# Performance work log

Measured on AMD Instinct MI355X. Metric: run time of the kernel, lower is better.

Reference implementation:

```python
import jax, jax.numpy as jnp
import numpy as np

N_ENTITIES = 100000
N_USERS = 50000
CHANNEL = 64
N_RELATIONS = 16
N_FACTORS = 4
N_EDGES = 1600000
N_INTER = 1000000


def setup_inputs() -> dict:
    key = jax.random.key(0)
    ks = jax.random.split(key, 11)
    return {
        "entity_emb": jax.random.normal(ks[0], (N_ENTITIES, CHANNEL), dtype=jnp.float32),
        "user_emb": jax.random.normal(ks[1], (N_USERS, CHANNEL), dtype=jnp.float32),
        "latent_emb": jax.random.normal(ks[2], (N_FACTORS, CHANNEL), dtype=jnp.float32),
        "weight": jax.random.normal(ks[3], (N_RELATIONS, CHANNEL), dtype=jnp.float32),
        "disen_weight_att": jax.random.normal(ks[4], (N_FACTORS, N_RELATIONS), dtype=jnp.float32),
        "interact_vals": jax.random.uniform(ks[5], (N_INTER,), dtype=jnp.float32),
        "head": jax.random.randint(ks[6], (N_EDGES,), 0, N_ENTITIES),
        "tail": jax.random.randint(ks[7], (N_EDGES,), 0, N_ENTITIES),
        # edge_type is 1-indexed in the original (weight[edge_type - 1])
        "edge_type": jax.random.randint(ks[8], (N_EDGES,), 1, N_RELATIONS + 1),
        "interact_rows": jax.random.randint(ks[9], (N_INTER,), 0, N_USERS),
        "interact_cols": jax.random.randint(ks[10], (N_INTER,), 0, N_ENTITIES),
    }


def reference(entity_emb, user_emb, latent_emb, weight, disen_weight_att,
              interact_vals, head, tail, edge_type, interact_rows, interact_cols):
    # ---- KG aggregate (GATED_ATT branch, vectorized; chunk loop is math-identical) ----
    rel = weight[edge_type - 1]                                  # [E, C]
    att = jax.nn.sigmoid(jnp.sum(entity_emb[head] * rel, axis=1))[:, None]  # [E, 1]
    neigh = att * (entity_emb[tail] * rel)                       # [E, C]
    seg_sum = jax.ops.segment_sum(neigh, head, num_segments=N_ENTITIES)     # [N_e, C]
    cnt = jax.ops.segment_sum(jnp.ones_like(att[:, 0]), head, num_segments=N_ENTITIES)
    entity_agg = seg_sum / jnp.maximum(cnt, 1.0)[:, None]        # scatter_mean (0 if empty)

    # ---- user aggregate ----
    score = jax.nn.softmax(user_emb @ latent_emb.T, axis=1)[:, :, None]      # [U, F, 1]
    user_agg = jax.ops.segment_sum(interact_vals[:, None] * entity_emb[interact_cols],
                                   interact_rows, num_segments=N_USERS)      # sparse mm
    disen = jax.nn.softmax(disen_weight_att, axis=-1) @ weight               # [F, C]
    gate = jnp.sum(disen[None, :, :] * score, axis=1)                        # [U, C]
    user_agg = user_agg * gate + user_agg
    return entity_agg, user_agg
```

## Files before the change

### kernel.cpp

```cpp
#include <hip/hip_runtime.h>

#define N_ENTITIES 100000
#define N_USERS 50000
#define CHANNEL 64
#define N_RELATIONS 16
#define N_FACTORS 4
#define N_EDGES 1600000
#define N_INTER 1000000
#define TMASK ((1 << 17) - 1)

#define BSH 6
#define BSZ 64
#define NBE 1563
#define NBU 782
#define CAP_E 1536
#define CAP_U 1792
#define TILE_E 4096
#define TILE_U 4096
#define NCONV 6250

typedef unsigned short u16;

__device__ __forceinline__ float wave_reduce_sum(float p) {
    #pragma unroll
    for (int off = 32; off > 0; off >>= 1) p += __shfl_xor(p, off);
    return p;
}

__device__ __forceinline__ int block_scan_incl(int v, int* wsum) {
    int lane = threadIdx.x & 63, wid = threadIdx.x >> 6;
    int x = v;
    #pragma unroll
    for (int off = 1; off < 64; off <<= 1) {
        int y = __shfl_up(x, off);
        if (lane >= off) x += y;
    }
    __syncthreads();
    if (lane == 63) wsum[wid] = x;
    __syncthreads();
    if (wid == 0) {
        int s = (lane < 16) ? wsum[lane] : 0;
        #pragma unroll
        for (int off = 1; off < 16; off <<= 1) {
            int y = __shfl_up(s, off);
            if (lane >= off) s += y;
        }
        if (lane < 16) wsum[lane] = s;
    }
    __syncthreads();
    return x + (wid ? wsum[wid - 1] : 0);
}

__device__ __forceinline__ u16 f32_to_bf16_rne(float x) {
    unsigned u = __float_as_uint(x);
    return (u16)((u + 0x7FFFu + ((u >> 16) & 1u)) >> 16);
}

template <bool BF16>
__device__ __forceinline__ float ldrow(const float* __restrict__ e32,
                                       const u16* __restrict__ e16,
                                       int row, int lane) {
    if (BF16) return __uint_as_float(((unsigned)e16[(size_t)row * CHANNEL + lane]) << 16);
    return e32[(size_t)row * CHANNEL + lane];
}

__device__ __forceinline__ void disen_body(const float* __restrict__ dwa,
                                           const float* __restrict__ weight,
                                           float* __restrict__ disen) {
    int f = threadIdx.x >> 6;
    int c = threadIdx.x & 63;
    float m = -INFINITY;
    #pragma unroll
    for (int r = 0; r < N_RELATIONS; ++r) m = fmaxf(m, dwa[f * N_RELATIONS + r]);
    float denom = 0.f, acc = 0.f;
    #pragma unroll
    for (int r = 0; r < N_RELATIONS; ++r) {
        float e = expf(dwa[f * N_RELATIONS + r] - m);
        denom += e;
        acc += e * weight[r * CHANNEL + c];
    }
    disen[f * CHANNEL + c] = acc / denom;
}

__global__ void disen_kernel(const float* __restrict__ dwa,
                             const float* __restrict__ weight,
                             float* __restrict__ disen) {
    disen_body(dwa, weight, disen);
}

__global__ __launch_bounds__(256) void conv_disen_kernel(
    const float* __restrict__ src, u16* __restrict__ dst,
    const float* __restrict__ dwa, const float* __restrict__ weight,
    float* __restrict__ disen) {
    if (blockIdx.x == NCONV) { disen_body(dwa, weight, disen); return; }
    int i = blockIdx.x * 256 + threadIdx.x;
    float4 v = ((const float4*)src)[i];
    ushort4 o;
    o.x = f32_to_bf16_rne(v.x);
    o.y = f32_to_bf16_rne(v.y);
    o.z = f32_to_bf16_rne(v.z);
    o.w = f32_to_bf16_rne(v.w);
    ((ushort4*)dst)[i] = o;
}

__global__ __launch_bounds__(1024) void hist_kernel(
    const int* __restrict__ head, const int* __restrict__ irows,
    int* __restrict__ wp_e, int* __restrict__ wp_u) {
    __shared__ int lh[NBE + NBU];
    int tid = threadIdx.x;
    for (int i = tid; i < NBE + NBU; i += 1024) lh[i] = 0;
    __syncthreads();
    const int NTOT = N_EDGES + N_INTER;
    for (int i = blockIdx.x * 1024 + tid; i < NTOT; i += gridDim.x * 1024) {
        if (i < N_EDGES) atomicAdd(&lh[head[i] >> BSH], 1);
        else             atomicAdd(&lh[NBE + (irows[i - N_EDGES] >> BSH)], 1);
    }
    __syncthreads();
    for (int i = tid; i < NBE + NBU; i += 1024) {
        int c = lh[i];
        if (c) {
            if (i < NBE) atomicAdd(&wp_e[i], c);
            else         atomicAdd(&wp_u[i - NBE], c);
        }
    }
}

__global__ __launch_bounds__(1024) void scan_kernel(
    int* __restrict__ wp_e, int* __restrict__ coff_e,
    int* __restrict__ wp_u, int* __restrict__ coff_u) {
    __shared__ int wsum[16];
    int tid = threadIdx.x;
    int c0 = wp_e[tid];
    int incl0 = block_scan_incl(c0, wsum);
    int tot0 = wsum[15];
    int i1 = 1024 + tid;
    int c1 = (i1 < NBE) ? wp_e[i1] : 0;
    int incl1 = block_scan_incl(c1, wsum) + tot0;
    int cu = (tid < NBU) ? wp_u[tid] : 0;
    int inclu = block_scan_incl(cu, wsum);
    { int ex = incl0 - c0; coff_e[tid] = ex; wp_e[tid] = ex; }
    if (i1 < NBE) { int ex = incl1 - c1; coff_e[i1] = ex; wp_e[i1] = ex; }
    if (tid == 0) coff_e[NBE] = N_EDGES;
    if (tid < NBU) { int ex = inclu - cu; coff_u[tid] = ex; wp_u[tid] = ex; }
    if (tid == 0) coff_u[NBU] = N_INTER;
}

__global__ __launch_bounds__(1024) void scatter_edge_kernel(
    const int* __restrict__ head, const int* __restrict__ tail,
    const int* __restrict__ etype,
    int* __restrict__ wp, int* __restrict__ pay_g) {
    __shared__ int s_hist[NBE], s_lofs[NBE], s_gbase[NBE];
    __shared__ int s_pay[TILE_E];
    __shared__ int s_dest[TILE_E];
    __shared__ int wsum[16];
    int tid = threadIdx.x;
    int g0 = blockIdx.x * TILE_E;
    int tilecnt = min(TILE_E, N_EDGES - g0);
    for (int i = tid; i < NBE; i += 1024) s_hist[i] = 0;
    int cb[4], pp[4], rk[4];
    __syncthreads();
    #pragma unroll
    for (int j = 0; j < 4; ++j) {
        int s = j * 1024 + tid;
        if (s < tilecnt) {
            int i = g0 + s;
            int h = head[i];
            cb[j] = h >> BSH;
            pp[j] = ((h & (BSZ - 1)) << 21) | ((etype[i] - 1) << 17) | tail[i];
        } else cb[j] = -1;
    }
    #pragma unroll
    for (int j = 0; j < 4; ++j)
        if (cb[j] >= 0) rk[j] = atomicAdd(&s_hist[cb[j]], 1);
    __syncthreads();
    int c0 = s_hist[tid];
    int incl0 = block_scan_incl(c0, wsum);
    int tot0 = wsum[15];
    int i1 = 1024 + tid;
    int c1 = (i1 < NBE) ? s_hist[i1] : 0;
    int incl1 = block_scan_incl(c1, wsum) + tot0;
    {
        int ex = incl0 - c0;
        s_lofs[tid] = ex;
        if (c0 > 0) s_gbase[tid] = atomicAdd(&wp[tid], c0) - ex;
    }
    if (i1 < NBE) {
        int ex = incl1 - c1;
        s_lofs[i1] = ex;
        if (c1 > 0) s_gbase[i1] = atomicAdd(&wp[i1], c1) - ex;
    }
    __syncthreads();
    #pragma unroll
    for (int j = 0; j < 4; ++j) {
        if (cb[j] >= 0) {
            int slot = s_lofs[cb[j]] + rk[j];
            s_pay[slot]  = pp[j];
            s_dest[slot] = s_gbase[cb[j]] + slot;
        }
    }
    __syncthreads();
    #pragma unroll
    for (int j = 0; j < 4; ++j) {
        int s = j * 1024 + tid;
        if (s < tilecnt) pay_g[s_dest[s]] = s_pay[s];
    }
}

__global__ __launch_bounds__(1024) void scatter_inter_kernel(
    const int* __restrict__ irows, const int* __restrict__ icols,
    const float* __restrict__ vals,
    int* __restrict__ wp, int* __restrict__ payA_g, float* __restrict__ payB_g) {
    __shared__ int s_hist[NBU], s_lofs[NBU], s_gbase[NBU];
    __shared__ int s_pay[TILE_U];
    __shared__ float s_val[TILE_U];
    __shared__ int s_dest[TILE_U];
    __shared__ int wsum[16];
    int tid = threadIdx.x;
    int g0 = blockIdx.x * TILE_U;
    int tilecnt = min(TILE_U, N_INTER - g0);
    for (int i = tid; i < NBU; i += 1024) s_hist[i] = 0;
    int cb[4], pp[4], rk[4];
    float vv[4];
    __syncthreads();
    #pragma unroll
    for (int j = 0; j < 4; ++j) {
        int s = j * 1024 + tid;
        if (s < tilecnt) {
            int i = g0 + s;
            int u = irows[i];
            cb[j] = u >> BSH;
            pp[j] = ((u & (BSZ - 1)) << 17) | icols[i];
            vv[j] = vals[i];
        } else cb[j] = -1;
    }
    #pragma unroll
    for (int j = 0; j < 4; ++j)
        if (cb[j] >= 0) rk[j] = atomicAdd(&s_hist[cb[j]], 1);
    __syncthreads();
    int c0 = (tid < NBU) ? s_hist[tid] : 0;
    int incl0 = block_scan_incl(c0, wsum);
    if (tid < NBU) {
        int ex = incl0 - c0;
        s_lofs[tid] = ex;
        if (c0 > 0) s_gbase[tid] = atomicAdd(&wp[tid], c0) - ex;
    }
    __syncthreads();
    #pragma unroll
    for (int j = 0; j < 4; ++j) {
        if (cb[j] >= 0) {
            int slot = s_lofs[cb[j]] + rk[j];
            s_pay[slot]  = pp[j];
            s_val[slot]  = vv[j];
            s_dest[slot] = s_gbase[cb[j]] + slot;
        }
    }
    __syncthreads();
    #pragma unroll
    for (int j = 0; j < 4; ++j) {
        int s = j * 1024 + tid;
        if (s < tilecnt) {
            payA_g[s_dest[s]] = s_pay[s];
            payB_g[s_dest[s]] = s_val[s];
        }
    }
}

template <bool BF16>
__global__ __launch_bounds__(256, 8) void gather_kernel(
    const float* __restrict__ entity_emb,
    const u16* __restrict__ emb16,
    const float* __restrict__ weight,
    const float* __restrict__ user_emb,
    const float* __restrict__ latent_emb,
    const float* __restrict__ disen,
    const int* __restrict__ coff_e,
    const int* __restrict__ pay_e,
    const int* __restrict__ coff_u,
    const int* __restrict__ payA_u,
    const float* __restrict__ payB_u,
    float* __restrict__ entity_agg,
    float* __restrict__ user_agg) {
    __shared__ __align__(16) char smem[16896];
    int tid = threadIdx.x;
    int wv = tid >> 6, lane = tid & 63;
    int bid = blockIdx.x;

    if (bid < NBE) {
        float* w65    = (float*)smem;
        float* s_attv = w65 + 1040;
        int*   s_pay  = (int*)(s_attv + 1024);
        int*   s_hist = s_pay + CAP_E;
        int*   s_scan = s_hist + 64;

        for (int i = tid; i < N_RELATIONS * CHANNEL; i += 256)
            w65[(i >> 6) * 65 + (i & 63)] = weight[i];
        if (tid < BSZ) s_hist[tid] = 0;
        int kbeg = coff_e[bid];
        int n = min(coff_e[bid + 1] - kbeg, CAP_E);
        __syncthreads();

        int myp[CAP_E / 256], myr[CAP_E / 256];
        #pragma unroll
        for (int j = 0; j < CAP_E / 256; ++j) {
            int s = j * 256 + tid;
            if (s < n) {
                int p = pay_e[kbeg + s];
                myp[j] = p;
                myr[j] = atomicAdd(&s_hist[p >> 21], 1);
            }
        }
        __syncthreads();
        if (wv == 0) {
            int x = s_hist[lane];
            #pragma unroll
            for (int off = 1; off < 64; off <<= 1) {
                int y = __shfl_up(x, off);
                if (lane >= off) x += y;
            }
            s_scan[lane] = x;
        }
        __syncthreads();
        #pragma unroll
        for (int j = 0; j < CAP_E / 256; ++j) {
            int s = j * 256 + tid;
            if (s < n) {
                int key = myp[j] >> 21;
                s_pay[s_scan[key] - s_hist[key] + myr[j]] = myp[j];
            }
        }

        int r = lane >> 2, q = lane & 3;
        for (int t = 0; t < 16; ++t) {
            int le = wv * 16 + t;
            int ge = bid * BSZ + le;
            if (ge >= N_ENTITIES) break;
            float eh = entity_emb[(size_t)ge * CHANNEL + lane];
            float p = 0.f;
            #pragma unroll
            for (int j = 0; j < 16; ++j)
                p += __shfl(eh, q * 16 + j) * w65[r * 65 + q * 16 + j];
            p += __shfl_xor(p, 1);
            p += __shfl_xor(p, 2);
            if (q == 0) s_attv[(le << 4) + r] = 1.f / (1.f + expf(-p));
        }
        __syncthreads();

        #define EBODY(K) { \
            int pp = s_pay[K]; \
            int et = (pp >> 17) & 15; \
            float v = ldrow<BF16>(entity_emb, emb16, pp & TMASK, lane); \
            acc += s_attv[(le << 4) + et] * v * w65[et * 65 + lane]; }
        for (int t = 0; t < 16; ++t) {
            int le = wv * 16 + t;
            int ge = bid * BSZ + le;
            if (ge >= N_ENTITIES) break;
            int cnt = s_hist[le];
            int ke = s_scan[le];
            int k = ke - cnt;
            float acc = 0.f;
            for (; k + 4 <= ke; k += 4) {
                EBODY(k); EBODY(k + 1); EBODY(k + 2); EBODY(k + 3);
            }
            for (; k < ke; ++k) EBODY(k);
            entity_agg[(size_t)ge * CHANNEL + lane] = acc / fmaxf((float)cnt, 1.0f);
        }
        #undef EBODY
    } else {
        int*   s_pay  = (int*)smem;
        float* s_val  = (float*)(s_pay + CAP_U);
        float* s_lat  = s_val + CAP_U;
        float* s_dis  = s_lat + 256;
        int*   s_hist = (int*)(s_dis + 256);
        int*   s_scan = s_hist + 64;

        if (tid < BSZ) s_hist[tid] = 0;
        if (tid < N_FACTORS * CHANNEL) {
            s_lat[tid] = latent_emb[tid];
            s_dis[tid] = disen[tid];
        }
        int b = bid - NBE;
        int kbeg = coff_u[b];
        int n = min(coff_u[b + 1] - kbeg, CAP_U);
        __syncthreads();

        int myp[CAP_U / 256], myr[CAP_U / 256];
        float myv[CAP_U / 256];
        #pragma unroll
        for (int j = 0; j < CAP_U / 256; ++j) {
            int s = j * 256 + tid;
            if (s < n) {
                int p = payA_u[kbeg + s];
                myp[j] = p;
                myv[j] = payB_u[kbeg + s];
                myr[j] = atomicAdd(&s_hist[p >> 17], 1);
            }
        }
        __syncthreads();
        if (wv == 0) {
            int x = s_hist[lane];
            #pragma unroll
            for (int off = 1; off < 64; off <<= 1) {
                int y = __shfl_up(x, off);
                if (lane >= off) x += y;
            }
            s_scan[lane] = x;
        }
        __syncthreads();
        #pragma unroll
        for (int j = 0; j < CAP_U / 256; ++j) {
            int s = j * 256 + tid;
            if (s < n) {
                int key = myp[j] >> 17;
                int slot = s_scan[key] - s_hist[key] + myr[j];
                s_pay[slot] = myp[j] & TMASK;
                s_val[slot] = myv[j];
            }
        }
        __syncthreads();

        #define UBODY(K) { \
            float v = ldrow<BF16>(entity_emb, emb16, s_pay[K], lane); \
            acc += s_val[K] * v; }
        for (int t = 0; t < 16; ++t) {
            int lu = wv * 16 + t;
            int gu = b * BSZ + lu;
            if (gu >= N_USERS) break;
            int cnt = s_hist[lu];
            int ke = s_scan[lu];
            int k = ke - cnt;
            float acc = 0.f;
            for (; k + 4 <= ke; k += 4) {
                UBODY(k); UBODY(k + 1); UBODY(k + 2); UBODY(k + 3);
            }
            for (; k < ke; ++k) UBODY(k);

            float ue = user_emb[(size_t)gu * CHANNEL + lane];
            float s[N_FACTORS];
            #pragma unroll
            for (int f = 0; f < N_FACTORS; ++f)
                s[f] = wave_reduce_sum(ue * s_lat[f * CHANNEL + lane]);
            float m = fmaxf(fmaxf(s[0], s[1]), fmaxf(s[2], s[3]));
            float d = 0.f;
            #pragma unroll
            for (int f = 0; f < N_FACTORS; ++f) { s[f] = expf(s[f] - m); d += s[f]; }
            float gate = 0.f;
            #pragma unroll
            for (int f = 0; f < N_FACTORS; ++f)
                gate += s_dis[f * CHANNEL + lane] * (s[f] / d);
            user_agg[(size_t)gu * CHANNEL + lane] = acc * gate + acc;
        }
        #undef UBODY
    }
}

extern "C" void kernel_launch(void* const* d_in, const int* in_sizes, int n_in,
                              void* d_out, int out_size, void* d_ws, size_t ws_size,
                              hipStream_t stream) {
    const float* entity_emb    = (const float*)d_in[0];
    const float* user_emb      = (const float*)d_in[1];
    const float* latent_emb    = (const float*)d_in[2];
    const float* weight        = (const float*)d_in[3];
    const float* dwa           = (const float*)d_in[4];
    const float* interact_vals = (const float*)d_in[5];
    const int*   head          = (const int*)d_in[6];
    const int*   tail          = (const int*)d_in[7];
    const int*   edge_type     = (const int*)d_in[8];
    const int*   irows         = (const int*)d_in[9];
    const int*   icols         = (const int*)d_in[10];

    float* entity_agg = (float*)d_out;
    float* user_agg   = (float*)d_out + (size_t)N_ENTITIES * CHANNEL;

    int*   wp_e   = (int*)d_ws;
    int*   wp_u   = wp_e + NBE;
    int*   coff_e = wp_u + NBU;
    int*   coff_u = coff_e + NBE + 1;
    int*   pay_e  = coff_u + NBU + 1;
    int*   payA_u = pay_e + N_EDGES;
    float* payB_u = (float*)(payA_u + N_INTER);
    float* disen  = payB_u + N_INTER;
    u16*   emb16  = (u16*)(disen + N_FACTORS * CHANNEL);

    size_t need_bf16 = (size_t)((char*)(emb16 + (size_t)N_ENTITIES * CHANNEL) - (char*)d_ws);
    bool use_bf16 = (ws_size >= need_bf16);
    if (!use_bf16) emb16 = (u16*)d_ws;

    hipMemsetAsync(wp_e, 0, (size_t)(NBE + NBU) * sizeof(int), stream);

    if (use_bf16) {
        conv_disen_kernel<<<NCONV + 1, 256, 0, stream>>>(
            entity_emb, emb16, dwa, weight, disen);
    } else {
        disen_kernel<<<1, 256, 0, stream>>>(dwa, weight, disen);
    }

    hist_kernel<<<128, 1024, 0, stream>>>(head, irows, wp_e, wp_u);
    scan_kernel<<<1, 1024, 0, stream>>>(wp_e, coff_e, wp_u, coff_u);

    scatter_edge_kernel<<<(N_EDGES + TILE_E - 1) / TILE_E, 1024, 0, stream>>>(
        head, tail, edge_type, wp_e, pay_e);
    scatter_inter_kernel<<<(N_INTER + TILE_U - 1) / TILE_U, 1024, 0, stream>>>(
        irows, icols, interact_vals, wp_u, payA_u, payB_u);

    if (use_bf16) {
        gather_kernel<true><<<NBE + NBU, 256, 0, stream>>>(
            entity_emb, emb16, weight, user_emb, latent_emb, disen,
            coff_e, pay_e, coff_u, payA_u, payB_u, entity_agg, user_agg);
    } else {
        gather_kernel<false><<<NBE + NBU, 256, 0, stream>>>(
            entity_emb, emb16, weight, user_emb, latent_emb, disen,
            coff_e, pay_e, coff_u, payA_u, payB_u, entity_agg, user_agg);
    }
}
```

Baseline: 201.2 us.

## Sort gather payloads by source-row chunk and fuse histogram into prep kernel

Inside each gather block, payloads are now bucketed by (source-entity chunk, destination row) instead of destination row alone. The gather loop walks the four 25000-row chunks in order, keeping 16 per-row accumulators in registers, so rows that are gathered concurrently fall in a narrower address range and should hit L2 more often. Separately, the histogram pass is merged into the bf16 conversion and disen kernel, which removes one launch. The cost is a 256-bucket scan, payloads read twice from global memory, more shared memory, and higher register pressure from the accumulator array.

```diff
diff --git a/kernel.cpp b/kernel.cpp
--- a/kernel.cpp
+++ b/kernel.cpp
@@ -18,6 +18,9 @@
 #define TILE_E 4096
 #define TILE_U 4096
 #define NCONV 6250
+#define NHIST 256
+#define NCHUNK 4
+#define CHUNK_ROWS 25000
 
 typedef unsigned short u16;
 
@@ -64,6 +67,27 @@
     return e32[(size_t)row * CHANNEL + lane];
 }
 
+__device__ __forceinline__ void scan256(const int* s_hist, int* s_scan,
+                                        int* s_wp, int* wtot) {
+    int tid = threadIdx.x;
+    int lane = tid & 63, wv = tid >> 6;
+    int c = s_hist[tid];
+    int x = c;
+    #pragma unroll
+    for (int off = 1; off < 64; off <<= 1) {
+        int y = __shfl_up(x, off);
+        if (lane >= off) x += y;
+    }
+    if (lane == 63) wtot[wv] = x;
+    __syncthreads();
+    if (wv >= 1) x += wtot[0];
+    if (wv >= 2) x += wtot[1];
+    if (wv >= 3) x += wtot[2];
+    s_scan[tid] = x;
+    s_wp[tid]   = x - c;
+    __syncthreads();
+}
+
 __device__ __forceinline__ void disen_body(const float* __restrict__ dwa,
                                            const float* __restrict__ weight,
                                            float* __restrict__ disen) {
@@ -88,19 +112,43 @@
     disen_body(dwa, weight, disen);
 }
 
-__global__ __launch_bounds__(256) void conv_disen_kernel(
+__global__ __launch_bounds__(256) void prep_kernel(
     const float* __restrict__ src, u16* __restrict__ dst,
     const float* __restrict__ dwa, const float* __restrict__ weight,
-    float* __restrict__ disen) {
-    if (blockIdx.x == NCONV) { disen_body(dwa, weight, disen); return; }
-    int i = blockIdx.x * 256 + threadIdx.x;
-    float4 v = ((const float4*)src)[i];
-    ushort4 o;
-    o.x = f32_to_bf16_rne(v.x);
-    o.y = f32_to_bf16_rne(v.y);
-    o.z = f32_to_bf16_rne(v.z);
-    o.w = f32_to_bf16_rne(v.w);
-    ((ushort4*)dst)[i] = o;
+    float* __restrict__ disen,
+    const int* __restrict__ head, const int* __restrict__ irows,
+    int* __restrict__ wp_e, int* __restrict__ wp_u) {
+    __shared__ int lh[NBE + NBU];
+    int bid = blockIdx.x;
+    int tid = threadIdx.x;
+    if (bid < NCONV) {
+        int i = bid * 256 + tid;
+        float4 v = ((const float4*)src)[i];
+        ushort4 o;
+        o.x = f32_to_bf16_rne(v.x);
+        o.y = f32_to_bf16_rne(v.y);
+        o.z = f32_to_bf16_rne(v.z);
+        o.w = f32_to_bf16_rne(v.w);
+        ((ushort4*)dst)[i] = o;
+        return;
+    }
+    if (bid == NCONV) { disen_body(dwa, weight, disen); return; }
+    for (int i = tid; i < NBE + NBU; i += 256) lh[i] = 0;
+    __syncthreads();
+    const int NTOT = N_EDGES + N_INTER;
+    int hb = bid - NCONV - 1;
+    for (int i = hb * 256 + tid; i < NTOT; i += NHIST * 256) {
+        if (i < N_EDGES) atomicAdd(&lh[head[i] >> BSH], 1);
+        else             atomicAdd(&lh[NBE + (irows[i - N_EDGES] >> BSH)], 1);
+    }
+    __syncthreads();
+    for (int i = tid; i < NBE + NBU; i += 256) {
+        int c = lh[i];
+        if (c) {
+            if (i < NBE) atomicAdd(&wp_e[i], c);
+            else         atomicAdd(&wp_u[i - NBE], c);
+        }
+    }
 }
 
 __global__ __launch_bounds__(1024) void hist_kernel(
@@ -280,7 +328,7 @@
     const float* __restrict__ payB_u,
     float* __restrict__ entity_agg,
     float* __restrict__ user_agg) {
-    __shared__ __align__(16) char smem[16896];
+    __shared__ __align__(16) char smem[19520];
     int tid = threadIdx.x;
     int wv = tid >> 6, lane = tid & 63;
     int bid = blockIdx.x;
@@ -290,43 +338,28 @@
         float* s_attv = w65 + 1040;
         int*   s_pay  = (int*)(s_attv + 1024);
         int*   s_hist = s_pay + CAP_E;
-        int*   s_scan = s_hist + 64;
+        int*   s_scan = s_hist + 256;
+        int*   s_wp   = s_scan + 256;
+        int*   wtot   = s_wp + 256;
 
         for (int i = tid; i < N_RELATIONS * CHANNEL; i += 256)
             w65[(i >> 6) * 65 + (i & 63)] = weight[i];
-        if (tid < BSZ) s_hist[tid] = 0;
+        s_hist[tid] = 0;
         int kbeg = coff_e[bid];
         int n = min(coff_e[bid + 1] - kbeg, CAP_E);
         __syncthreads();
 
-        int myp[CAP_E / 256], myr[CAP_E / 256];
-        #pragma unroll
-        for (int j = 0; j < CAP_E / 256; ++j) {
-            int s = j * 256 + tid;
-            if (s < n) {
-                int p = pay_e[kbeg + s];
-                myp[j] = p;
-                myr[j] = atomicAdd(&s_hist[p >> 21], 1);
-            }
+        for (int s = tid; s < n; s += 256) {
+            int p = pay_e[kbeg + s];
+            int key = ((int)((unsigned)(p & TMASK) / CHUNK_ROWS) << 6) | (p >> 21);
+            atomicAdd(&s_hist[key], 1);
         }
         __syncthreads();
-        if (wv == 0) {
-            int x = s_hist[lane];
-            #pragma unroll
-            for (int off = 1; off < 64; off <<= 1) {
-                int y = __shfl_up(x, off);
-                if (lane >= off) x += y;
-            }
-            s_scan[lane] = x;
-        }
-        __syncthreads();
-        #pragma unroll
-        for (int j = 0; j < CAP_E / 256; ++j) {
-            int s = j * 256 + tid;
-            if (s < n) {
-                int key = myp[j] >> 21;
-                s_pay[s_scan[key] - s_hist[key] + myr[j]] = myp[j];
-            }
+        scan256(s_hist, s_scan, s_wp, wtot);
+        for (int s = tid; s < n; s += 256) {
+            int p = pay_e[kbeg + s];
+            int key = ((int)((unsigned)(p & TMASK) / CHUNK_ROWS) << 6) | (p >> 21);
+            s_pay[atomicAdd(&s_wp[key], 1)] = p;
         }
 
         int r = lane >> 2, q = lane & 3;
@@ -345,35 +378,62 @@
         }
         __syncthreads();
 
-        #define EBODY(K) { \
-            int pp = s_pay[K]; \
-            int et = (pp >> 17) & 15; \
-            float v = ldrow<BF16>(entity_emb, emb16, pp & TMASK, lane); \
-            acc += s_attv[(le << 4) + et] * v * w65[et * 65 + lane]; }
+        float acc[16];
+        #pragma unroll
+        for (int t = 0; t < 16; ++t) acc[t] = 0.f;
+
+        for (int c = 0; c < NCHUNK; ++c) {
+            #pragma unroll
+            for (int t = 0; t < 16; ++t) {
+                int le = wv * 16 + t;
+                int key = (c << 6) | le;
+                int ke = s_scan[key];
+                int k = ke - s_hist[key];
+                float a = acc[t];
+                for (; k + 4 <= ke; k += 4) {
+                    int p0 = s_pay[k], p1 = s_pay[k + 1];
+                    int p2 = s_pay[k + 2], p3 = s_pay[k + 3];
+                    float v0 = ldrow<BF16>(entity_emb, emb16, p0 & TMASK, lane);
+                    float v1 = ldrow<BF16>(entity_emb, emb16, p1 & TMASK, lane);
+                    float v2 = ldrow<BF16>(entity_emb, emb16, p2 & TMASK, lane);
+                    float v3 = ldrow<BF16>(entity_emb, emb16, p3 & TMASK, lane);
+                    int e0 = (p0 >> 17) & 15, e1 = (p1 >> 17) & 15;
+                    int e2 = (p2 >> 17) & 15, e3 = (p3 >> 17) & 15;
+                    a += s_attv[(le << 4) + e0] * v0 * w65[e0 * 65 + lane];
+                    a += s_attv[(le << 4) + e1] * v1 * w65[e1 * 65 + lane];
+                    a += s_attv[(le << 4) + e2] * v2 * w65[e2 * 65 + lane];
+                    a += s_attv[(le << 4) + e3] * v3 * w65[e3 * 65 + lane];
+                }
+                for (; k < ke; ++k) {
+                    int p0 = s_pay[k];
+                    int e0 = (p0 >> 17) & 15;
+                    float v0 = ldrow<BF16>(entity_emb, emb16, p0 & TMASK, lane);
+                    a += s_attv[(le << 4) + e0] * v0 * w65[e0 * 65 + lane];
+                }
+                acc[t] = a;
+            }
+        }
+
+        #pragma unroll
         for (int t = 0; t < 16; ++t) {
             int le = wv * 16 + t;
             int ge = bid * BSZ + le;
-            if (ge >= N_ENTITIES) break;
-            int cnt = s_hist[le];
-            int ke = s_scan[le];
-            int k = ke - cnt;
-            float acc = 0.f;
-            for (; k + 4 <= ke; k += 4) {
-                EBODY(k); EBODY(k + 1); EBODY(k + 2); EBODY(k + 3);
+            if (ge < N_ENTITIES) {
+                int deg = s_hist[le] + s_hist[64 + le] + s_hist[128 + le] + s_hist[192 + le];
+                entity_agg[(size_t)ge * CHANNEL + lane] = acc[t] / fmaxf((float)deg, 1.0f);
             }
-            for (; k < ke; ++k) EBODY(k);
-            entity_agg[(size_t)ge * CHANNEL + lane] = acc / fmaxf((float)cnt, 1.0f);
-        }
-        #undef EBODY
+        }
     } else {
         int*   s_pay  = (int*)smem;
         float* s_val  = (float*)(s_pay + CAP_U);
         float* s_lat  = s_val + CAP_U;
         float* s_dis  = s_lat + 256;
         int*   s_hist = (int*)(s_dis + 256);
-        int*   s_scan = s_hist + 64;
-
-        if (tid < BSZ) s_hist[tid] = 0;
+        int*   s_scan = s_hist + 256;
+        int*   s_wp   = s_scan + 256;
+        int*   wtot   = s_wp + 256;
+
+        s_hist[tid] = 0;
         if (tid < N_FACTORS * CHANNEL) {
             s_lat[tid] = latent_emb[tid];
             s_dis[tid] = disen[tid];
@@ -383,73 +443,68 @@
         int n = min(coff_u[b + 1] - kbeg, CAP_U);
         __syncthreads();
 
-        int myp[CAP_U / 256], myr[CAP_U / 256];
-        float myv[CAP_U / 256];
+        for (int s = tid; s < n; s += 256) {
+            int p = payA_u[kbeg + s];
+            int key = ((int)((unsigned)(p & TMASK) / CHUNK_ROWS) << 6) | (p >> 17);
+            atomicAdd(&s_hist[key], 1);
+        }
+        __syncthreads();
+        scan256(s_hist, s_scan, s_wp, wtot);
+        for (int s = tid; s < n; s += 256) {
+            int p = payA_u[kbeg + s];
+            int key = ((int)((unsigned)(p & TMASK) / CHUNK_ROWS) << 6) | (p >> 17);
+            int slot = atomicAdd(&s_wp[key], 1);
+            s_pay[slot] = p & TMASK;
+            s_val[slot] = payB_u[kbeg + s];
+        }
+        __syncthreads();
+
+        float acc[16];
         #pragma unroll
-        for (int j = 0; j < CAP_U / 256; ++j) {
-            int s = j * 256 + tid;
-            if (s < n) {
-                int p = payA_u[kbeg + s];
-                myp[j] = p;
-                myv[j] = payB_u[kbeg + s];
-                myr[j] = atomicAdd(&s_hist[p >> 17], 1);
+        for (int t = 0; t < 16; ++t) acc[t] = 0.f;
+
+        for (int c = 0; c < NCHUNK; ++c) {
+            #pragma unroll
+            for (int t = 0; t < 16; ++t) {
+                int lu = wv * 16 + t;
+                int key = (c << 6) | lu;
+                int ke = s_scan[key];
+                int k = ke - s_hist[key];
+                float a = acc[t];
+                for (; k + 4 <= ke; k += 4) {
+                    float v0 = ldrow<BF16>(entity_emb, emb16, s_pay[k],     lane);
+                    float v1 = ldrow<BF16>(entity_emb, emb16, s_pay[k + 1], lane);
+                    float v2 = ldrow<BF16>(entity_emb, emb16, s_pay[k + 2], lane);
+                    float v3 = ldrow<BF16>(entity_emb, emb16, s_pay[k + 3], lane);
+                    a += s_val[k] * v0 + s_val[k + 1] * v1 + s_val[k + 2] * v2 + s_val[k + 3] * v3;
+                }
+                for (; k < ke; ++k)
+                    a += s_val[k] * ldrow<BF16>(entity_emb, emb16, s_pay[k], lane);
+                acc[t] = a;
             }
         }
-        __syncthreads();
-        if (wv == 0) {
-            int x = s_hist[lane];
-            #pragma unroll
-            for (int off = 1; off < 64; off <<= 1) {
-                int y = __shfl_up(x, off);
-                if (lane >= off) x += y;
-            }
-            s_scan[lane] = x;
-        }
-        __syncthreads();
+
         #pragma unroll
-        for (int j = 0; j < CAP_U / 256; ++j) {
-            int s = j * 256 + tid;
-            if (s < n) {
-                int key = myp[j] >> 17;
-                int slot = s_scan[key] - s_hist[key] + myr[j];
-                s_pay[slot] = myp[j] & TMASK;
-                s_val[slot] = myv[j];
-            }
-        }
-        __syncthreads();
-
-        #define UBODY(K) { \
-            float v = ldrow<BF16>(entity_emb, emb16, s_pay[K], lane); \
-            acc += s_val[K] * v; }
         for (int t = 0; t < 16; ++t) {
             int lu = wv * 16 + t;
             int gu = b * BSZ + lu;
-            if (gu >= N_USERS) break;
-            int cnt = s_hist[lu];
-            int ke = s_scan[lu];
-            int k = ke - cnt;
-            float acc = 0.f;
-            for (; k + 4 <= ke; k += 4) {
-                UBODY(k); UBODY(k + 1); UBODY(k + 2); UBODY(k + 3);
+            if (gu < N_USERS) {
+                float ue = user_emb[(size_t)gu * CHANNEL + lane];
+                float s[N_FACTORS];
+                #pragma unroll
+                for (int f = 0; f < N_FACTORS; ++f)
+                    s[f] = wave_reduce_sum(ue * s_lat[f * CHANNEL + lane]);
+                float m = fmaxf(fmaxf(s[0], s[1]), fmaxf(s[2], s[3]));
+                float d = 0.f;
+                #pragma unroll
+                for (int f = 0; f < N_FACTORS; ++f) { s[f] = expf(s[f] - m); d += s[f]; }
+                float gate = 0.f;
+                #pragma unroll
+                for (int f = 0; f < N_FACTORS; ++f)
+                    gate += s_dis[f * CHANNEL + lane] * (s[f] / d);
+                user_agg[(size_t)gu * CHANNEL + lane] = acc[t] * gate + acc[t];
             }
-            for (; k < ke; ++k) UBODY(k);
-
-            float ue = user_emb[(size_t)gu * CHANNEL + lane];
-            float s[N_FACTORS];
-            #pragma unroll
-            for (int f = 0; f < N_FACTORS; ++f)
-                s[f] = wave_reduce_sum(ue * s_lat[f * CHANNEL + lane]);
-            float m = fmaxf(fmaxf(s[0], s[1]), fmaxf(s[2], s[3]));
-            float d = 0.f;
-            #pragma unroll
-            for (int f = 0; f < N_FACTORS; ++f) { s[f] = expf(s[f] - m); d += s[f]; }
-            float gate = 0.f;
-            #pragma unroll
-            for (int f = 0; f < N_FACTORS; ++f)
-                gate += s_dis[f * CHANNEL + lane] * (s[f] / d);
-            user_agg[(size_t)gu * CHANNEL + lane] = acc * gate + acc;
-        }
-        #undef UBODY
+        }
     }
 }
 
@@ -488,13 +543,13 @@
     hipMemsetAsync(wp_e, 0, (size_t)(NBE + NBU) * sizeof(int), stream);
 
     if (use_bf16) {
-        conv_disen_kernel<<<NCONV + 1, 256, 0, stream>>>(
-            entity_emb, emb16, dwa, weight, disen);
+        prep_kernel<<<NCONV + 1 + NHIST, 256, 0, stream>>>(
+            entity_emb, emb16, dwa, weight, disen, head, irows, wp_e, wp_u);
     } else {
         disen_kernel<<<1, 256, 0, stream>>>(dwa, weight, disen);
-    }
-
-    hist_kernel<<<128, 1024, 0, stream>>>(head, irows, wp_e, wp_u);
+        hist_kernel<<<128, 1024, 0, stream>>>(head, irows, wp_e, wp_u);
+    }
+
     scan_kernel<<<1, 1024, 0, stream>>>(wp_e, coff_e, wp_u, coff_u);
 
     scatter_edge_kernel<<<(N_EDGES + TILE_E - 1) / TILE_E, 1024, 0, stream>>>(
```

Measured after the change: 242.9 us. 20.7% more time.

## Fuse histogram into prep kernel, merge scatters, bf16 head loads, nontemporal stores

Applied to the files above, without the earlier changes.

Folds the bucket histogram into the bf16 conversion/disen prep kernel, so the histogram runs alongside the conversion and one launch disappears. The two scatter kernels become a single launch that branches on block index, sharing a dynamically carved shared-memory buffer. The gather now loads the head entity row through the bf16 path, and outputs are written with nontemporal stores. The aim is fewer launches, more concurrency between independent stages and less memory traffic. The costs are a larger shared-memory footprint per scatter block and bf16 rounding of the head embedding used in the attention dot product.

```diff
diff --git a/kernel.cpp b/kernel.cpp
--- a/kernel.cpp
+++ b/kernel.cpp
@@ -17,7 +17,10 @@
 #define CAP_U 1792
 #define TILE_E 4096
 #define TILE_U 4096
+#define NTBE 391
+#define NTBU 245
 #define NCONV 6250
+#define NHIST 256
 
 typedef unsigned short u16;
 
@@ -88,19 +91,43 @@
     disen_body(dwa, weight, disen);
 }
 
-__global__ __launch_bounds__(256) void conv_disen_kernel(
+__global__ __launch_bounds__(256) void prep_kernel(
     const float* __restrict__ src, u16* __restrict__ dst,
     const float* __restrict__ dwa, const float* __restrict__ weight,
-    float* __restrict__ disen) {
-    if (blockIdx.x == NCONV) { disen_body(dwa, weight, disen); return; }
-    int i = blockIdx.x * 256 + threadIdx.x;
-    float4 v = ((const float4*)src)[i];
-    ushort4 o;
-    o.x = f32_to_bf16_rne(v.x);
-    o.y = f32_to_bf16_rne(v.y);
-    o.z = f32_to_bf16_rne(v.z);
-    o.w = f32_to_bf16_rne(v.w);
-    ((ushort4*)dst)[i] = o;
+    float* __restrict__ disen,
+    const int* __restrict__ head, const int* __restrict__ irows,
+    int* __restrict__ wp_e, int* __restrict__ wp_u) {
+    __shared__ int lh[NBE + NBU];
+    int bid = blockIdx.x;
+    int tid = threadIdx.x;
+    if (bid < NCONV) {
+        int i = bid * 256 + tid;
+        float4 v = ((const float4*)src)[i];
+        ushort4 o;
+        o.x = f32_to_bf16_rne(v.x);
+        o.y = f32_to_bf16_rne(v.y);
+        o.z = f32_to_bf16_rne(v.z);
+        o.w = f32_to_bf16_rne(v.w);
+        ((ushort4*)dst)[i] = o;
+        return;
+    }
+    if (bid == NCONV) { disen_body(dwa, weight, disen); return; }
+    for (int i = tid; i < NBE + NBU; i += 256) lh[i] = 0;
+    __syncthreads();
+    const int NTOT = N_EDGES + N_INTER;
+    int hb = bid - NCONV - 1;
+    for (int i = hb * 256 + tid; i < NTOT; i += NHIST * 256) {
+        if (i < N_EDGES) atomicAdd(&lh[head[i] >> BSH], 1);
+        else             atomicAdd(&lh[NBE + (irows[i - N_EDGES] >> BSH)], 1);
+    }
+    __syncthreads();
+    for (int i = tid; i < NBE + NBU; i += 256) {
+        int c = lh[i];
+        if (c) {
+            if (i < NBE) atomicAdd(&wp_e[i], c);
+            else         atomicAdd(&wp_u[i - NBE], c);
+        }
+    }
 }
 
 __global__ __launch_bounds__(1024) void hist_kernel(
@@ -145,122 +172,127 @@
     if (tid == 0) coff_u[NBU] = N_INTER;
 }
 
-__global__ __launch_bounds__(1024) void scatter_edge_kernel(
+__global__ __launch_bounds__(1024) void scatter_kernel(
     const int* __restrict__ head, const int* __restrict__ tail,
     const int* __restrict__ etype,
-    int* __restrict__ wp, int* __restrict__ pay_g) {
-    __shared__ int s_hist[NBE], s_lofs[NBE], s_gbase[NBE];
-    __shared__ int s_pay[TILE_E];
-    __shared__ int s_dest[TILE_E];
+    const int* __restrict__ irows, const int* __restrict__ icols,
+    const float* __restrict__ vals,
+    int* __restrict__ wp_e, int* __restrict__ pay_e,
+    int* __restrict__ wp_u, int* __restrict__ payA_u, float* __restrict__ payB_u) {
+    __shared__ __align__(16) char smem[58624];
     __shared__ int wsum[16];
     int tid = threadIdx.x;
-    int g0 = blockIdx.x * TILE_E;
-    int tilecnt = min(TILE_E, N_EDGES - g0);
-    for (int i = tid; i < NBE; i += 1024) s_hist[i] = 0;
-    int cb[4], pp[4], rk[4];
-    __syncthreads();
-    #pragma unroll
-    for (int j = 0; j < 4; ++j) {
-        int s = j * 1024 + tid;
-        if (s < tilecnt) {
-            int i = g0 + s;
-            int h = head[i];
-            cb[j] = h >> BSH;
-            pp[j] = ((h & (BSZ - 1)) << 21) | ((etype[i] - 1) << 17) | tail[i];
-        } else cb[j] = -1;
-    }
-    #pragma unroll
-    for (int j = 0; j < 4; ++j)
-        if (cb[j] >= 0) rk[j] = atomicAdd(&s_hist[cb[j]], 1);
-    __syncthreads();
-    int c0 = s_hist[tid];
-    int incl0 = block_scan_incl(c0, wsum);
-    int tot0 = wsum[15];
-    int i1 = 1024 + tid;
-    int c1 = (i1 < NBE) ? s_hist[i1] : 0;
-    int incl1 = block_scan_incl(c1, wsum) + tot0;
-    {
-        int ex = incl0 - c0;
-        s_lofs[tid] = ex;
-        if (c0 > 0) s_gbase[tid] = atomicAdd(&wp[tid], c0) - ex;
-    }
-    if (i1 < NBE) {
-        int ex = incl1 - c1;
-        s_lofs[i1] = ex;
-        if (c1 > 0) s_gbase[i1] = atomicAdd(&wp[i1], c1) - ex;
-    }
-    __syncthreads();
-    #pragma unroll
-    for (int j = 0; j < 4; ++j) {
-        if (cb[j] >= 0) {
-            int slot = s_lofs[cb[j]] + rk[j];
-            s_pay[slot]  = pp[j];
-            s_dest[slot] = s_gbase[cb[j]] + slot;
-        }
-    }
-    __syncthreads();
-    #pragma unroll
-    for (int j = 0; j < 4; ++j) {
-        int s = j * 1024 + tid;
-        if (s < tilecnt) pay_g[s_dest[s]] = s_pay[s];
-    }
-}
-
-__global__ __launch_bounds__(1024) void scatter_inter_kernel(
-    const int* __restrict__ irows, const int* __restrict__ icols,
-    const float* __restrict__ vals,
-    int* __restrict__ wp, int* __restrict__ payA_g, float* __restrict__ payB_g) {
-    __shared__ int s_hist[NBU], s_lofs[NBU], s_gbase[NBU];
-    __shared__ int s_pay[TILE_U];
-    __shared__ float s_val[TILE_U];
-    __shared__ int s_dest[TILE_U];
-    __shared__ int wsum[16];
-    int tid = threadIdx.x;
-    int g0 = blockIdx.x * TILE_U;
-    int tilecnt = min(TILE_U, N_INTER - g0);
-    for (int i = tid; i < NBU; i += 1024) s_hist[i] = 0;
-    int cb[4], pp[4], rk[4];
-    float vv[4];
-    __syncthreads();
-    #pragma unroll
-    for (int j = 0; j < 4; ++j) {
-        int s = j * 1024 + tid;
-        if (s < tilecnt) {
-            int i = g0 + s;
-            int u = irows[i];
-            cb[j] = u >> BSH;
-            pp[j] = ((u & (BSZ - 1)) << 17) | icols[i];
-            vv[j] = vals[i];
-        } else cb[j] = -1;
-    }
-    #pragma unroll
-    for (int j = 0; j < 4; ++j)
-        if (cb[j] >= 0) rk[j] = atomicAdd(&s_hist[cb[j]], 1);
-    __syncthreads();
-    int c0 = (tid < NBU) ? s_hist[tid] : 0;
-    int incl0 = block_scan_incl(c0, wsum);
-    if (tid < NBU) {
-        int ex = incl0 - c0;
-        s_lofs[tid] = ex;
-        if (c0 > 0) s_gbase[tid] = atomicAdd(&wp[tid], c0) - ex;
-    }
-    __syncthreads();
-    #pragma unroll
-    for (int j = 0; j < 4; ++j) {
-        if (cb[j] >= 0) {
-            int slot = s_lofs[cb[j]] + rk[j];
-            s_pay[slot]  = pp[j];
-            s_val[slot]  = vv[j];
-            s_dest[slot] = s_gbase[cb[j]] + slot;
-        }
-    }
-    __syncthreads();
-    #pragma unroll
-    for (int j = 0; j < 4; ++j) {
-        int s = j * 1024 + tid;
-        if (s < tilecnt) {
-            payA_g[s_dest[s]] = s_pay[s];
-            payB_g[s_dest[s]] = s_val[s];
+    int bid = blockIdx.x;
+
+    if (bid < NTBE) {
+        int* s_hist  = (int*)smem;
+        int* s_lofs  = s_hist + NBE;
+        int* s_gbase = s_lofs + NBE;
+        int* s_pay   = s_gbase + NBE;
+        int* s_dest  = s_pay + TILE_E;
+        int g0 = bid * TILE_E;
+        int tilecnt = min(TILE_E, N_EDGES - g0);
+        for (int i = tid; i < NBE; i += 1024) s_hist[i] = 0;
+        int cb[4], pp[4], rk[4];
+        __syncthreads();
+        #pragma unroll
+        for (int j = 0; j < 4; ++j) {
+            int s = j * 1024 + tid;
+            if (s < tilecnt) {
+                int i = g0 + s;
+                int h = head[i];
+                cb[j] = h >> BSH;
+                pp[j] = ((h & (BSZ - 1)) << 21) | ((etype[i] - 1) << 17) | tail[i];
+            } else cb[j] = -1;
+        }
+        #pragma unroll
+        for (int j = 0; j < 4; ++j)
+            if (cb[j] >= 0) rk[j] = atomicAdd(&s_hist[cb[j]], 1);
+        __syncthreads();
+        int c0 = s_hist[tid];
+        int incl0 = block_scan_incl(c0, wsum);
+        int tot0 = wsum[15];
+        int i1 = 1024 + tid;
+        int c1 = (i1 < NBE) ? s_hist[i1] : 0;
+        int incl1 = block_scan_incl(c1, wsum) + tot0;
+        {
+            int ex = incl0 - c0;
+            s_lofs[tid] = ex;
+            if (c0 > 0) s_gbase[tid] = atomicAdd(&wp_e[tid], c0) - ex;
+        }
+        if (i1 < NBE) {
+            int ex = incl1 - c1;
+            s_lofs[i1] = ex;
+            if (c1 > 0) s_gbase[i1] = atomicAdd(&wp_e[i1], c1) - ex;
+        }
+        __syncthreads();
+        #pragma unroll
+        for (int j = 0; j < 4; ++j) {
+            if (cb[j] >= 0) {
+                int slot = s_lofs[cb[j]] + rk[j];
+                s_pay[slot]  = pp[j];
+                s_dest[slot] = s_gbase[cb[j]] + slot;
+            }
+        }
+        __syncthreads();
+        #pragma unroll
+        for (int j = 0; j < 4; ++j) {
+            int s = j * 1024 + tid;
+            if (s < tilecnt) pay_e[s_dest[s]] = s_pay[s];
+        }
+    } else {
+        int*   s_hist  = (int*)smem;
+        int*   s_lofs  = s_hist + NBU;
+        int*   s_gbase = s_lofs + NBU;
+        int*   s_pay   = s_gbase + NBU;
+        float* s_val   = (float*)(s_pay + TILE_U);
+        int*   s_dest  = (int*)(s_val + TILE_U);
+        int g0 = (bid - NTBE) * TILE_U;
+        int tilecnt = min(TILE_U, N_INTER - g0);
+        for (int i = tid; i < NBU; i += 1024) s_hist[i] = 0;
+        int cb[4], pp[4], rk[4];
+        float vv[4];
+        __syncthreads();
+        #pragma unroll
+        for (int j = 0; j < 4; ++j) {
+            int s = j * 1024 + tid;
+            if (s < tilecnt) {
+                int i = g0 + s;
+                int u = irows[i];
+                cb[j] = u >> BSH;
+                pp[j] = ((u & (BSZ - 1)) << 17) | icols[i];
+                vv[j] = vals[i];
+            } else cb[j] = -1;
+        }
+        #pragma unroll
+        for (int j = 0; j < 4; ++j)
+            if (cb[j] >= 0) rk[j] = atomicAdd(&s_hist[cb[j]], 1);
+        __syncthreads();
+        int c0 = (tid < NBU) ? s_hist[tid] : 0;
+        int incl0 = block_scan_incl(c0, wsum);
+        if (tid < NBU) {
+            int ex = incl0 - c0;
+            s_lofs[tid] = ex;
+            if (c0 > 0) s_gbase[tid] = atomicAdd(&wp_u[tid], c0) - ex;
+        }
+        __syncthreads();
+        #pragma unroll
+        for (int j = 0; j < 4; ++j) {
+            if (cb[j] >= 0) {
+                int slot = s_lofs[cb[j]] + rk[j];
+                s_pay[slot]  = pp[j];
+                s_val[slot]  = vv[j];
+                s_dest[slot] = s_gbase[cb[j]] + slot;
+            }
+        }
+        __syncthreads();
+        #pragma unroll
+        for (int j = 0; j < 4; ++j) {
+            int s = j * 1024 + tid;
+            if (s < tilecnt) {
+                payA_u[s_dest[s]] = s_pay[s];
+                payB_u[s_dest[s]] = s_val[s];
+            }
         }
     }
 }
@@ -334,7 +366,7 @@
             int le = wv * 16 + t;
             int ge = bid * BSZ + le;
             if (ge >= N_ENTITIES) break;
-            float eh = entity_emb[(size_t)ge * CHANNEL + lane];
+            float eh = ldrow<BF16>(entity_emb, emb16, ge, lane);
             float p = 0.f;
             #pragma unroll
             for (int j = 0; j < 16; ++j)
@@ -362,7 +394,8 @@
                 EBODY(k); EBODY(k + 1); EBODY(k + 2); EBODY(k + 3);
             }
             for (; k < ke; ++k) EBODY(k);
-            entity_agg[(size_t)ge * CHANNEL + lane] = acc / fmaxf((float)cnt, 1.0f);
+            __builtin_nontemporal_store(acc / fmaxf((float)cnt, 1.0f),
+                                        &entity_agg[(size_t)ge * CHANNEL + lane]);
         }
         #undef EBODY
     } else {
@@ -447,7 +480,8 @@
             #pragma unroll
             for (int f = 0; f < N_FACTORS; ++f)
                 gate += s_dis[f * CHANNEL + lane] * (s[f] / d);
-            user_agg[(size_t)gu * CHANNEL + lane] = acc * gate + acc;
+            __builtin_nontemporal_store(acc * gate + acc,
+                                        &user_agg[(size_t)gu * CHANNEL + lane]);
         }
         #undef UBODY
     }
@@ -488,19 +522,18 @@
     hipMemsetAsync(wp_e, 0, (size_t)(NBE + NBU) * sizeof(int), stream);
 
     if (use_bf16) {
-        conv_disen_kernel<<<NCONV + 1, 256, 0, stream>>>(
-            entity_emb, emb16, dwa, weight, disen);
+        prep_kernel<<<NCONV + 1 + NHIST, 256, 0, stream>>>(
+            entity_emb, emb16, dwa, weight, disen, head, irows, wp_e, wp_u);
     } else {
         disen_kernel<<<1, 256, 0, stream>>>(dwa, weight, disen);
-    }
-
-    hist_kernel<<<128, 1024, 0, stream>>>(head, irows, wp_e, wp_u);
+        hist_kernel<<<128, 1024, 0, stream>>>(head, irows, wp_e, wp_u);
+    }
+
     scan_kernel<<<1, 1024, 0, stream>>>(wp_e, coff_e, wp_u, coff_u);
 
-    scatter_edge_kernel<<<(N_EDGES + TILE_E - 1) / TILE_E, 1024, 0, stream>>>(
-        head, tail, edge_type, wp_e, pay_e);
-    scatter_inter_kernel<<<(N_INTER + TILE_U - 1) / TILE_U, 1024, 0, stream>>>(
-        irows, icols, interact_vals, wp_u, payA_u, payB_u);
+    scatter_kernel<<<NTBE + NTBU, 1024, 0, stream>>>(
+        head, tail, edge_type, irows, icols, interact_vals,
+        wp_e, pay_e, wp_u, payA_u, payB_u);
 
     if (use_bf16) {
         gather_kernel<true><<<NBE + NBU, 256, 0, stream>>>(
```

Result: no change. 199.3 us, median of 2 (-0.9%).
